# Optimization experiments

Measured on AMD Instinct MI355X. Metric: run time of the kernel, lower is better.

Reference implementation:

```python
import jax, jax.numpy as jnp
import numpy as np

N_EMBED = 1024
HEAD_SIZE = 64


def setup_inputs() -> dict:
    key = jax.random.key(0)
    kx, kq, kk, kv = jax.random.split(key, 4)
    x = jax.random.normal(kx, (8, 2048, N_EMBED), dtype=jnp.float32)
    s = 1.0 / np.sqrt(N_EMBED)
    # nn.Linear weights are [out, in]; store as [in, out] for x @ W
    W_q = jax.random.uniform(kq, (N_EMBED, HEAD_SIZE), jnp.float32, -s, s)
    W_k = jax.random.uniform(kk, (N_EMBED, HEAD_SIZE), jnp.float32, -s, s)
    W_v = jax.random.uniform(kv, (N_EMBED, HEAD_SIZE), jnp.float32, -s, s)
    return {"x": x, "W_q": W_q, "W_k": W_k, "W_v": W_v}


def reference(x, W_q, W_k, W_v):
    b, t, c = x.shape
    q = x @ W_q  # [b, t, h]
    k = x @ W_k
    v = x @ W_v
    scale = k.shape[-1] ** -0.5
    wei = jnp.einsum("bqh,bkh->bqk", q, k) * scale  # [b, t, t]
    causal = jnp.tril(jnp.ones((t, t), dtype=bool))
    wei = jnp.where(causal, wei, -jnp.inf)
    wei = jax.nn.softmax(wei, axis=-1)
    # dropout p=0.0 -> identity
    return jnp.einsum("bqk,bkh->bqh", wei, v)
```

## Files before the change

### kernel.cpp

```cpp
#include <hip/hip_runtime.h>
#include <math.h>

typedef unsigned short u16;
typedef unsigned int u32;
typedef __attribute__((ext_vector_type(4))) float f32x4;
typedef __attribute__((ext_vector_type(8))) short s16x8;
typedef __attribute__((ext_vector_type(4))) unsigned short u16x4;

#define T_ 2048
#define C_ 1024

__device__ __forceinline__ u16 f2b(float f) {
  u32 u = __builtin_bit_cast(u32, f);
  return (u16)((u + 0x8000u) >> 16);
}

__device__ __forceinline__ s16x8 pack8v(f32x4 a, f32x4 b) {
  s16x8 r;
  r[0] = (short)f2b(a[0]); r[1] = (short)f2b(a[1]);
  r[2] = (short)f2b(a[2]); r[3] = (short)f2b(a[3]);
  r[4] = (short)f2b(b[0]); r[5] = (short)f2b(b[1]);
  r[6] = (short)f2b(b[2]); r[7] = (short)f2b(b[3]);
  return r;
}

__device__ __forceinline__ void gld_lds16(const void* g, void* l) {
  __builtin_amdgcn_global_load_lds(
      (const __attribute__((address_space(1))) u32*)g,
      (__attribute__((address_space(3))) u32*)l, 16, 0, 0);
}

__global__ __launch_bounds__(256) void wconv(const float* __restrict__ Wq,
                                             const float* __restrict__ Wk,
                                             const float* __restrict__ Wv,
                                             u16* __restrict__ Wt) {
  __shared__ u16 t[64][68];
  const int bm = blockIdx.x >> 4;
  const int kt = blockIdx.x & 15;
  const float* src = (bm == 0) ? Wq : ((bm == 1) ? Wk : Wv);
  const float scale = (bm == 0) ? 0.18033688f : 1.0f;
  const int krow = threadIdx.x >> 2;
  const int c0 = (threadIdx.x & 3) * 16;
  const float* sp = src + (size_t)(kt * 64 + krow) * 64 + c0;
#pragma unroll
  for (int i = 0; i < 4; ++i) {
    float4 v = *(const float4*)(sp + i * 4);
    t[c0 + i * 4 + 0][krow] = f2b(v.x * scale);
    t[c0 + i * 4 + 1][krow] = f2b(v.y * scale);
    t[c0 + i * 4 + 2][krow] = f2b(v.z * scale);
    t[c0 + i * 4 + 3][krow] = f2b(v.w * scale);
  }
  __syncthreads();
  const int n = threadIdx.x >> 2;
  const int koff = (threadIdx.x & 3) * 16;
  u16* dst = Wt + (size_t)(bm * 64 + n) * C_ + kt * 64 + koff;
#pragma unroll
  for (int i = 0; i < 4; ++i)
    *(u16x4*)(dst + i * 4) = *(const u16x4*)(&t[n][koff + i * 4]);
}

__global__ __launch_bounds__(256, 2) void proj(const float* __restrict__ x,
                                               const u16* __restrict__ Wt,
                                               u16* __restrict__ qo,
                                               u16* __restrict__ ko,
                                               u16* __restrict__ vt) {
  __shared__ __align__(16) float xs[32 * 64];
  __shared__ __align__(16) u16 wsh[192 * 64];
  const int tid = threadIdx.x;
  const int wave = tid >> 6, lane = tid & 63;
  const int quad = lane >> 4, l15 = lane & 15;
  const int mg = wave >> 1, nh = wave & 1;
  const int m0 = blockIdx.x * 32;

  const int xrow_in = lane >> 4;
  const int xslot = lane & 15;
  const int wrow_in = lane >> 3;
  const int wg = (lane & 7) ^ wrow_in;

  f32x4 acc[6];
#pragma unroll
  for (int j = 0; j < 6; ++j) acc[j] = {0.f, 0.f, 0.f, 0.f};

  for (int kt = 0; kt < 16; ++kt) {
#pragma unroll
    for (int c = 0; c < 2; ++c) {
      const int row = 8 * wave + 4 * c + xrow_in;
      const int g = xslot ^ (row & 15);
      gld_lds16(x + (size_t)(m0 + row) * C_ + kt * 64 + g * 4,
                &xs[(8 * wave + 4 * c) * 64]);
    }
#pragma unroll
    for (int c = 0; c < 6; ++c) {
      const int row = (6 * wave + c) * 8 + wrow_in;
      gld_lds16(Wt + (size_t)row * C_ + kt * 64 + wg * 8,
                &wsh[(6 * wave + c) * 8 * 64]);
    }
    __syncthreads();
    s16x8 af[2];
#pragma unroll
    for (int ks = 0; ks < 2; ++ks) {
      const int row = 16 * mg + l15;
      const int cc = ks * 8 + quad * 2;
      f32x4 p0 = *(const f32x4*)&xs[row * 64 + ((cc ^ (row & 15)) * 4)];
      f32x4 p1 = *(const f32x4*)&xs[row * 64 + (((cc + 1) ^ (row & 15)) * 4)];
      af[ks] = pack8v(p0, p1);
    }
#pragma unroll
    for (int jj = 0; jj < 6; ++jj) {
      const int row = (nh * 6 + jj) * 16 + l15;
#pragma unroll
      for (int ks = 0; ks < 2; ++ks) {
        const int cc = ks * 4 + quad;
        s16x8 bf = *(const s16x8*)&wsh[row * 64 + ((cc ^ (row & 7)) * 8)];
        acc[jj] = __builtin_amdgcn_mfma_f32_16x16x32_bf16(af[ks], bf, acc[jj], 0, 0, 0);
      }
    }
    __syncthreads();
  }

  const int r0 = m0 + 16 * mg + quad * 4;
#pragma unroll
  for (int jj = 0; jj < 6; ++jj) {
    const int ns = nh * 6 + jj;
    if (ns < 4) {
      const int col = ns * 16 + l15;
#pragma unroll
      for (int i = 0; i < 4; ++i)
        qo[(size_t)(r0 + i) * 64 + col] = f2b(acc[jj][i]);
    } else if (ns < 8) {
      const int col = (ns - 4) * 16 + l15;
#pragma unroll
      for (int i = 0; i < 4; ++i)
        ko[(size_t)(r0 + i) * 64 + col] = f2b(acc[jj][i]);
    } else {
      const int d = (ns - 8) * 16 + l15;
      const int bb = r0 >> 11, t0 = r0 & 2047;
      u16x4 pk = {f2b(acc[jj][0]), f2b(acc[jj][1]), f2b(acc[jj][2]), f2b(acc[jj][3])};
      *(u16x4*)(vt + (size_t)bb * (64 * T_) + (size_t)d * T_ + t0) = pk;
    }
  }
}

__global__ __launch_bounds__(256, 4) void attn(const u16* __restrict__ qw,
                                               const u16* __restrict__ kw,
                                               const u16* __restrict__ vt,
                                               float* __restrict__ out) {
  __shared__ __align__(16) u16 Pb[4][16 * 72];
  __shared__ float mbuf[4][16];
  __shared__ float lbuf[4][16];
  const int tid = threadIdx.x;
  const int wave = tid >> 6, lane = tid & 63;
  const int quad = lane >> 4, l15 = lane & 15;
  const int b = blockIdx.x & 7;
  const int qt = 127 - (blockIdx.x >> 3);

  const u16* qp = qw + ((size_t)b * T_ + qt * 16) * 64;
  const u16* kb = kw + (size_t)b * T_ * 64;
  const u16* vb = vt + (size_t)b * 64 * T_;

  s16x8 qf[2];
#pragma unroll
  for (int ks = 0; ks < 2; ++ks)
    qf[ks] = *(const s16x8*)(qp + l15 * 64 + ks * 32 + quad * 8);

  f32x4 o[4];
#pragma unroll
  for (int m = 0; m < 4; ++m) o[m] = {0.f, 0.f, 0.f, 0.f};
  float mr = -INFINITY, lr = 0.0f;

  u16* P = Pb[wave];
  const int jd = qt >> 2;

  for (int j = wave; j <= jd; j += 4) {
    const u16* kp = kb + (size_t)j * 64 * 64;
    const u16* vp = vb + j * 64;
    s16x8 kf[2][4], vf[2][4];
#pragma unroll
    for (int ks = 0; ks < 2; ++ks)
#pragma unroll
      for (int m = 0; m < 4; ++m)
        kf[ks][m] = *(const s16x8*)(kp + (16 * m + l15) * 64 + ks * 32 + quad * 8);
#pragma unroll
    for (int ks = 0; ks < 2; ++ks)
#pragma unroll
      for (int m = 0; m < 4; ++m)
        vf[ks][m] = *(const s16x8*)(vp + (size_t)(16 * m + l15) * T_ + ks * 32 + quad * 8);

    f32x4 s[4];
#pragma unroll
    for (int m = 0; m < 4; ++m) s[m] = {0.f, 0.f, 0.f, 0.f};
#pragma unroll
    for (int ks = 0; ks < 2; ++ks)
#pragma unroll
      for (int m = 0; m < 4; ++m)
        s[m] = __builtin_amdgcn_mfma_f32_16x16x32_bf16(kf[ks][m], qf[ks], s[m], 0, 0, 0);

    if (j == jd) {
#pragma unroll
      for (int m = 0; m < 4; ++m)
#pragma unroll
        for (int i = 0; i < 4; ++i)
          if (64 * jd + 16 * m + quad * 4 + i > 16 * qt + l15) s[m][i] = -INFINITY;
    }
    float mt = s[0][0];
#pragma unroll
    for (int m = 0; m < 4; ++m)
#pragma unroll
      for (int i = 0; i < 4; ++i) mt = fmaxf(mt, s[m][i]);
    mt = fmaxf(mt, __shfl_xor(mt, 16));
    mt = fmaxf(mt, __shfl_xor(mt, 32));
    const float mn = fmaxf(mr, mt);
    const float al = exp2f(mr - mn);
    mr = mn;
    float rs = 0.0f;
#pragma unroll
    for (int m = 0; m < 4; ++m)
#pragma unroll
      for (int i = 0; i < 4; ++i) {
        float p = exp2f(s[m][i] - mn);
        s[m][i] = p;
        rs += p;
      }
    rs += __shfl_xor(rs, 16);
    rs += __shfl_xor(rs, 32);
    lr = lr * al + rs;
#pragma unroll
    for (int m = 0; m < 4; ++m) {
      u16x4 pk = {f2b(s[m][0]), f2b(s[m][1]), f2b(s[m][2]), f2b(s[m][3])};
      *(u16x4*)(&P[l15 * 72 + 16 * m + quad * 4]) = pk;
    }
#pragma unroll
    for (int m = 0; m < 4; ++m) o[m] *= al;
#pragma unroll
    for (int ks = 0; ks < 2; ++ks) {
      s16x8 pf = *(const s16x8*)(&P[l15 * 72 + ks * 32 + quad * 8]);
#pragma unroll
      for (int m = 0; m < 4; ++m)
        o[m] = __builtin_amdgcn_mfma_f32_16x16x32_bf16(vf[ks][m], pf, o[m], 0, 0, 0);
    }
  }
  if (quad == 0) {
    mbuf[wave][l15] = mr;
    lbuf[wave][l15] = lr;
  }
#pragma unroll
  for (int m = 0; m < 4; ++m) {
    u16x4 pk = {f2b(o[m][0]), f2b(o[m][1]), f2b(o[m][2]), f2b(o[m][3])};
    *(u16x4*)(&Pb[wave][l15 * 72 + 16 * m + quad * 4]) = pk;
  }
  __syncthreads();
  const int r = tid >> 4;
  const int cg = (tid & 15) * 4;
  float fw[4];
  float mstar = -INFINITY, lsum = 0.0f;
#pragma unroll
  for (int w = 0; w < 4; ++w) mstar = fmaxf(mstar, mbuf[w][r]);
#pragma unroll
  for (int w = 0; w < 4; ++w) {
    fw[w] = exp2f(mbuf[w][r] - mstar);
    lsum += fw[w] * lbuf[w][r];
  }
  const float inv = 1.0f / lsum;
  float a0 = 0.f, a1 = 0.f, a2 = 0.f, a3 = 0.f;
#pragma unroll
  for (int w = 0; w < 4; ++w) {
    u16x4 vv = *(const u16x4*)(&Pb[w][r * 72 + cg]);
    a0 += fw[w] * __builtin_bit_cast(float, ((u32)vv[0]) << 16);
    a1 += fw[w] * __builtin_bit_cast(float, ((u32)vv[1]) << 16);
    a2 += fw[w] * __builtin_bit_cast(float, ((u32)vv[2]) << 16);
    a3 += fw[w] * __builtin_bit_cast(float, ((u32)vv[3]) << 16);
  }
  float4 st = {a0 * inv, a1 * inv, a2 * inv, a3 * inv};
  *(float4*)(out + ((size_t)b * T_ + qt * 16 + r) * 64 + cg) = st;
}

extern "C" void kernel_launch(void* const* d_in, const int* in_sizes, int n_in,
                              void* d_out, int out_size, void* d_ws, size_t ws_size,
                              hipStream_t stream) {
  const float* x  = (const float*)d_in[0];
  const float* Wq = (const float*)d_in[1];
  const float* Wk = (const float*)d_in[2];
  const float* Wv = (const float*)d_in[3];
  float* out = (float*)d_out;
  char* ws = (char*)d_ws;
  u16* Wt = (u16*)ws;
  u16* q  = (u16*)(ws + 393216);
  u16* k  = (u16*)(ws + 393216 + 2097152);
  u16* vT = (u16*)(ws + 393216 + 2 * 2097152);
  hipLaunchKernelGGL(wconv, dim3(48), dim3(256), 0, stream, Wq, Wk, Wv, Wt);
  hipLaunchKernelGGL(proj, dim3(512), dim3(256), 0, stream, x, Wt, q, k, vT);
  hipLaunchKernelGGL(attn, dim3(1024), dim3(256), 0, stream, q, k, vT, out);
}
```

Measured before the change: 151.8 us.

## Double-buffer projection and restructure attention into split-KV with LDS-staged tiles and merge

The projection kernel now uses 512-thread blocks over 64 rows, converts x to bf16 once into LDS, and double-buffers both the x and W tiles so the next k-tile loads while MFMAs run. The attention kernel now gives each block 64 queries (one 16-row slice per wave) and stages shared K/V tiles into double-buffered LDS. The KV range is split into two halves per query tile, and a new merge kernel combines the two partial outputs. This is meant to reduce redundant global K/V loads and balance the causal workload, at the cost of an extra launch and a round trip of fp32 partials through global memory.

```diff
diff --git a/kernel.cpp b/kernel.cpp
--- a/kernel.cpp
+++ b/kernel.cpp
@@ -15,12 +15,12 @@
   return (u16)((u + 0x8000u) >> 16);
 }
 
-__device__ __forceinline__ s16x8 pack8v(f32x4 a, f32x4 b) {
+__device__ __forceinline__ s16x8 pack8(float4 a, float4 b) {
   s16x8 r;
-  r[0] = (short)f2b(a[0]); r[1] = (short)f2b(a[1]);
-  r[2] = (short)f2b(a[2]); r[3] = (short)f2b(a[3]);
-  r[4] = (short)f2b(b[0]); r[5] = (short)f2b(b[1]);
-  r[6] = (short)f2b(b[2]); r[7] = (short)f2b(b[3]);
+  r[0] = (short)f2b(a.x); r[1] = (short)f2b(a.y);
+  r[2] = (short)f2b(a.z); r[3] = (short)f2b(a.w);
+  r[4] = (short)f2b(b.x); r[5] = (short)f2b(b.y);
+  r[6] = (short)f2b(b.z); r[7] = (short)f2b(b.w);
   return r;
 }
 
@@ -59,62 +59,75 @@
     *(u16x4*)(dst + i * 4) = *(const u16x4*)(&t[n][koff + i * 4]);
 }
 
-__global__ __launch_bounds__(256, 2) void proj(const float* __restrict__ x,
+__global__ __launch_bounds__(512, 2) void proj(const float* __restrict__ x,
                                                const u16* __restrict__ Wt,
                                                u16* __restrict__ qo,
                                                u16* __restrict__ ko,
                                                u16* __restrict__ vt) {
-  __shared__ __align__(16) float xs[32 * 64];
-  __shared__ __align__(16) u16 wsh[192 * 64];
+  __shared__ __align__(16) u16 xs[2][64 * 64];
+  __shared__ __align__(16) u16 wsh[2][192 * 64];
   const int tid = threadIdx.x;
   const int wave = tid >> 6, lane = tid & 63;
   const int quad = lane >> 4, l15 = lane & 15;
   const int mg = wave >> 1, nh = wave & 1;
-  const int m0 = blockIdx.x * 32;
-
-  const int xrow_in = lane >> 4;
-  const int xslot = lane & 15;
-  const int wrow_in = lane >> 3;
-  const int wg = (lane & 7) ^ wrow_in;
+  const int m0 = blockIdx.x * 64;
+
+  const int rin = lane >> 3, slot = lane & 7;
+  const int xrow = tid >> 3, xcg = (tid & 7) * 8;
+  const float* xp = x + (size_t)(m0 + xrow) * C_ + xcg;
+  const int xslot = (tid & 7) ^ (xrow & 7);
+
+  auto stageW = [&](int kt, int buf) {
+#pragma unroll
+    for (int c = 0; c < 3; ++c) {
+      const int row0 = 24 * wave + 8 * c;
+      const int g = slot ^ rin;
+      gld_lds16(Wt + (size_t)(row0 + rin) * C_ + kt * 64 + g * 8,
+                &wsh[buf][row0 * 64]);
+    }
+  };
 
   f32x4 acc[6];
 #pragma unroll
   for (int j = 0; j < 6; ++j) acc[j] = {0.f, 0.f, 0.f, 0.f};
 
+  stageW(0, 0);
+  {
+    float4 p0 = *(const float4*)(xp);
+    float4 p1 = *(const float4*)(xp + 4);
+    *(s16x8*)(&xs[0][xrow * 64 + xslot * 8]) = pack8(p0, p1);
+  }
+  __syncthreads();
+
   for (int kt = 0; kt < 16; ++kt) {
-#pragma unroll
-    for (int c = 0; c < 2; ++c) {
-      const int row = 8 * wave + 4 * c + xrow_in;
-      const int g = xslot ^ (row & 15);
-      gld_lds16(x + (size_t)(m0 + row) * C_ + kt * 64 + g * 4,
-                &xs[(8 * wave + 4 * c) * 64]);
-    }
-#pragma unroll
-    for (int c = 0; c < 6; ++c) {
-      const int row = (6 * wave + c) * 8 + wrow_in;
-      gld_lds16(Wt + (size_t)row * C_ + kt * 64 + wg * 8,
-                &wsh[(6 * wave + c) * 8 * 64]);
-    }
-    __syncthreads();
+    const int buf = kt & 1;
+    float4 p0, p1;
+    if (kt < 15) {
+      stageW(kt + 1, buf ^ 1);
+      p0 = *(const float4*)(xp + (kt + 1) * 64);
+      p1 = *(const float4*)(xp + (kt + 1) * 64 + 4);
+    }
     s16x8 af[2];
-#pragma unroll
-    for (int ks = 0; ks < 2; ++ks) {
-      const int row = 16 * mg + l15;
-      const int cc = ks * 8 + quad * 2;
-      f32x4 p0 = *(const f32x4*)&xs[row * 64 + ((cc ^ (row & 15)) * 4)];
-      f32x4 p1 = *(const f32x4*)&xs[row * 64 + (((cc + 1) ^ (row & 15)) * 4)];
-      af[ks] = pack8v(p0, p1);
+    {
+      const int r = 16 * mg + l15;
+#pragma unroll
+      for (int ks = 0; ks < 2; ++ks) {
+        const int sl = (ks * 4 + quad) ^ (l15 & 7);
+        af[ks] = *(const s16x8*)&xs[buf][r * 64 + sl * 8];
+      }
     }
 #pragma unroll
     for (int jj = 0; jj < 6; ++jj) {
-      const int row = (nh * 6 + jj) * 16 + l15;
+      const int R = (nh * 6 + jj) * 16 + l15;
 #pragma unroll
       for (int ks = 0; ks < 2; ++ks) {
-        const int cc = ks * 4 + quad;
-        s16x8 bf = *(const s16x8*)&wsh[row * 64 + ((cc ^ (row & 7)) * 8)];
+        const int sl = (ks * 4 + quad) ^ (l15 & 7);
+        s16x8 bf = *(const s16x8*)&wsh[buf][R * 64 + sl * 8];
         acc[jj] = __builtin_amdgcn_mfma_f32_16x16x32_bf16(af[ks], bf, acc[jj], 0, 0, 0);
       }
     }
+    if (kt < 15)
+      *(s16x8*)(&xs[buf ^ 1][xrow * 64 + xslot * 8]) = pack8(p0, p1);
     __syncthreads();
   }
 
@@ -141,23 +154,27 @@
   }
 }
 
-__global__ __launch_bounds__(256, 4) void attn(const u16* __restrict__ qw,
+__global__ __launch_bounds__(256, 2) void attn(const u16* __restrict__ qw,
                                                const u16* __restrict__ kw,
                                                const u16* __restrict__ vt,
-                                               float* __restrict__ out) {
+                                               float* __restrict__ opart,
+                                               float2* __restrict__ ml) {
+  __shared__ __align__(16) u16 kvb[2][2][4096];
   __shared__ __align__(16) u16 Pb[4][16 * 72];
-  __shared__ float mbuf[4][16];
-  __shared__ float lbuf[4][16];
   const int tid = threadIdx.x;
   const int wave = tid >> 6, lane = tid & 63;
   const int quad = lane >> 4, l15 = lane & 15;
   const int b = blockIdx.x & 7;
-  const int qt = 127 - (blockIdx.x >> 3);
-
-  const u16* qp = qw + ((size_t)b * T_ + qt * 16) * 64;
+  const int h = (blockIdx.x >> 3) & 1;
+  const int qt = 31 - (blockIdx.x >> 4);
+
+  const u16* qp = qw + ((size_t)b * T_ + qt * 64 + 16 * wave) * 64;
   const u16* kb = kw + (size_t)b * T_ * 64;
   const u16* vb = vt + (size_t)b * 64 * T_;
 
+  const int n = qt + 1, c = (n + 1) >> 1;
+  const int j0 = h ? c : 0, j1 = h ? n : c;
+
   s16x8 qf[2];
 #pragma unroll
   for (int ks = 0; ks < 2; ++ks)
@@ -166,112 +183,131 @@
   f32x4 o[4];
 #pragma unroll
   for (int m = 0; m < 4; ++m) o[m] = {0.f, 0.f, 0.f, 0.f};
-  float mr = -INFINITY, lr = 0.0f;
-
+  float mr = -1e30f, lr = 0.0f;
+
+  const int rin = lane >> 3, slot = lane & 7;
+  const int g8 = slot ^ rin;
   u16* P = Pb[wave];
-  const int jd = qt >> 2;
-
-  for (int j = wave; j <= jd; j += 4) {
-    const u16* kp = kb + (size_t)j * 64 * 64;
-    const u16* vp = vb + j * 64;
-    s16x8 kf[2][4], vf[2][4];
-#pragma unroll
-    for (int ks = 0; ks < 2; ++ks)
+
+  auto stage = [&](int j, int buf) {
+    if (wave < 2) {
+#pragma unroll
+      for (int cc = 0; cc < 4; ++cc) {
+        const int r0 = 32 * wave + 8 * cc;
+        gld_lds16(kb + (size_t)(64 * j + r0 + rin) * 64 + g8 * 8,
+                  &kvb[buf][0][r0 * 64]);
+      }
+    } else {
+#pragma unroll
+      for (int cc = 0; cc < 4; ++cc) {
+        const int r0 = 32 * (wave - 2) + 8 * cc;
+        gld_lds16(vb + (size_t)(r0 + rin) * T_ + 64 * j + g8 * 8,
+                  &kvb[buf][1][r0 * 64]);
+      }
+    }
+  };
+
+  if (j0 < j1) {
+    stage(j0, 0);
+    __syncthreads();
+    for (int j = j0; j < j1; ++j) {
+      const int buf = (j - j0) & 1;
+      if (j + 1 < j1) stage(j + 1, buf ^ 1);
+      const u16* Kt = kvb[buf][0];
+      const u16* Vt = kvb[buf][1];
+      f32x4 s[4];
+#pragma unroll
+      for (int m = 0; m < 4; ++m) s[m] = {0.f, 0.f, 0.f, 0.f};
+#pragma unroll
+      for (int ks = 0; ks < 2; ++ks)
+#pragma unroll
+        for (int m = 0; m < 4; ++m) {
+          const int row = 16 * m + l15;
+          const int sl = (ks * 4 + quad) ^ (l15 & 7);
+          s16x8 kf = *(const s16x8*)&Kt[row * 64 + sl * 8];
+          s[m] = __builtin_amdgcn_mfma_f32_16x16x32_bf16(kf, qf[ks], s[m], 0, 0, 0);
+        }
+      if (j == qt) {
+#pragma unroll
+        for (int m = 0; m < 4; ++m)
+#pragma unroll
+          for (int i = 0; i < 4; ++i)
+            if (16 * m + quad * 4 + i > 16 * wave + l15) s[m][i] = -INFINITY;
+      }
+      float mt = s[0][0];
 #pragma unroll
       for (int m = 0; m < 4; ++m)
-        kf[ks][m] = *(const s16x8*)(kp + (16 * m + l15) * 64 + ks * 32 + quad * 8);
-#pragma unroll
-    for (int ks = 0; ks < 2; ++ks)
+#pragma unroll
+        for (int i = 0; i < 4; ++i) mt = fmaxf(mt, s[m][i]);
+      mt = fmaxf(mt, __shfl_xor(mt, 16));
+      mt = fmaxf(mt, __shfl_xor(mt, 32));
+      const float mn = fmaxf(mr, mt);
+      const float al = exp2f(mr - mn);
+      mr = mn;
+      float rs = 0.0f;
 #pragma unroll
       for (int m = 0; m < 4; ++m)
-        vf[ks][m] = *(const s16x8*)(vp + (size_t)(16 * m + l15) * T_ + ks * 32 + quad * 8);
-
-    f32x4 s[4];
-#pragma unroll
-    for (int m = 0; m < 4; ++m) s[m] = {0.f, 0.f, 0.f, 0.f};
-#pragma unroll
-    for (int ks = 0; ks < 2; ++ks)
-#pragma unroll
-      for (int m = 0; m < 4; ++m)
-        s[m] = __builtin_amdgcn_mfma_f32_16x16x32_bf16(kf[ks][m], qf[ks], s[m], 0, 0, 0);
-
-    if (j == jd) {
-#pragma unroll
-      for (int m = 0; m < 4; ++m)
-#pragma unroll
-        for (int i = 0; i < 4; ++i)
-          if (64 * jd + 16 * m + quad * 4 + i > 16 * qt + l15) s[m][i] = -INFINITY;
-    }
-    float mt = s[0][0];
-#pragma unroll
-    for (int m = 0; m < 4; ++m)
-#pragma unroll
-      for (int i = 0; i < 4; ++i) mt = fmaxf(mt, s[m][i]);
-    mt = fmaxf(mt, __shfl_xor(mt, 16));
-    mt = fmaxf(mt, __shfl_xor(mt, 32));
-    const float mn = fmaxf(mr, mt);
-    const float al = exp2f(mr - mn);
-    mr = mn;
-    float rs = 0.0f;
-#pragma unroll
-    for (int m = 0; m < 4; ++m)
-#pragma unroll
-      for (int i = 0; i < 4; ++i) {
-        float p = exp2f(s[m][i] - mn);
-        s[m][i] = p;
-        rs += p;
-      }
-    rs += __shfl_xor(rs, 16);
-    rs += __shfl_xor(rs, 32);
-    lr = lr * al + rs;
-#pragma unroll
-    for (int m = 0; m < 4; ++m) {
-      u16x4 pk = {f2b(s[m][0]), f2b(s[m][1]), f2b(s[m][2]), f2b(s[m][3])};
-      *(u16x4*)(&P[l15 * 72 + 16 * m + quad * 4]) = pk;
-    }
-#pragma unroll
-    for (int m = 0; m < 4; ++m) o[m] *= al;
-#pragma unroll
-    for (int ks = 0; ks < 2; ++ks) {
-      s16x8 pf = *(const s16x8*)(&P[l15 * 72 + ks * 32 + quad * 8]);
-#pragma unroll
-      for (int m = 0; m < 4; ++m)
-        o[m] = __builtin_amdgcn_mfma_f32_16x16x32_bf16(vf[ks][m], pf, o[m], 0, 0, 0);
-    }
-  }
-  if (quad == 0) {
-    mbuf[wave][l15] = mr;
-    lbuf[wave][l15] = lr;
-  }
-#pragma unroll
-  for (int m = 0; m < 4; ++m) {
-    u16x4 pk = {f2b(o[m][0]), f2b(o[m][1]), f2b(o[m][2]), f2b(o[m][3])};
-    *(u16x4*)(&Pb[wave][l15 * 72 + 16 * m + quad * 4]) = pk;
-  }
-  __syncthreads();
-  const int r = tid >> 4;
-  const int cg = (tid & 15) * 4;
-  float fw[4];
-  float mstar = -INFINITY, lsum = 0.0f;
-#pragma unroll
-  for (int w = 0; w < 4; ++w) mstar = fmaxf(mstar, mbuf[w][r]);
-#pragma unroll
-  for (int w = 0; w < 4; ++w) {
-    fw[w] = exp2f(mbuf[w][r] - mstar);
-    lsum += fw[w] * lbuf[w][r];
-  }
-  const float inv = 1.0f / lsum;
-  float a0 = 0.f, a1 = 0.f, a2 = 0.f, a3 = 0.f;
-#pragma unroll
-  for (int w = 0; w < 4; ++w) {
-    u16x4 vv = *(const u16x4*)(&Pb[w][r * 72 + cg]);
-    a0 += fw[w] * __builtin_bit_cast(float, ((u32)vv[0]) << 16);
-    a1 += fw[w] * __builtin_bit_cast(float, ((u32)vv[1]) << 16);
-    a2 += fw[w] * __builtin_bit_cast(float, ((u32)vv[2]) << 16);
-    a3 += fw[w] * __builtin_bit_cast(float, ((u32)vv[3]) << 16);
-  }
-  float4 st = {a0 * inv, a1 * inv, a2 * inv, a3 * inv};
-  *(float4*)(out + ((size_t)b * T_ + qt * 16 + r) * 64 + cg) = st;
+#pragma unroll
+        for (int i = 0; i < 4; ++i) {
+          float p = exp2f(s[m][i] - mn);
+          s[m][i] = p;
+          rs += p;
+        }
+      rs += __shfl_xor(rs, 16);
+      rs += __shfl_xor(rs, 32);
+      lr = lr * al + rs;
+#pragma unroll
+      for (int m = 0; m < 4; ++m) {
+        u16x4 pk = {f2b(s[m][0]), f2b(s[m][1]), f2b(s[m][2]), f2b(s[m][3])};
+        *(u16x4*)(&P[l15 * 72 + 16 * m + quad * 4]) = pk;
+      }
+#pragma unroll
+      for (int m = 0; m < 4; ++m) o[m] *= al;
+#pragma unroll
+      for (int ks = 0; ks < 2; ++ks) {
+        s16x8 pf = *(const s16x8*)(&P[l15 * 72 + ks * 32 + quad * 8]);
+#pragma unroll
+        for (int m = 0; m < 4; ++m) {
+          const int row = 16 * m + l15;
+          const int sl = (ks * 4 + quad) ^ (l15 & 7);
+          s16x8 vf = *(const s16x8*)&Vt[row * 64 + sl * 8];
+          o[m] = __builtin_amdgcn_mfma_f32_16x16x32_bf16(vf, pf, o[m], 0, 0, 0);
+        }
+      }
+      __syncthreads();
+    }
+  }
+  const int pidx = ((b * 32 + qt) * 2 + h);
+  float* OP = opart + (size_t)pidx * 4096;
+  const int qloc = 16 * wave + l15;
+#pragma unroll
+  for (int m = 0; m < 4; ++m)
+    *(f32x4*)(&OP[qloc * 64 + 16 * m + quad * 4]) = o[m];
+  if (quad == 0) ml[pidx * 64 + qloc] = {mr, lr};
+}
+
+__global__ __launch_bounds__(256) void merge(const float* __restrict__ opart,
+                                             const float2* __restrict__ ml,
+                                             float* __restrict__ out) {
+  const int blk = blockIdx.x;
+  const int b = blk >> 5, qt = blk & 31;
+  const int t = threadIdx.x;
+  const int r = t >> 2, cg = (t & 3) * 16;
+  const float2 ml0 = ml[(blk * 2 + 0) * 64 + r];
+  const float2 ml1 = ml[(blk * 2 + 1) * 64 + r];
+  const float mstar = fmaxf(ml0.x, ml1.x);
+  const float f0 = exp2f(ml0.x - mstar), f1 = exp2f(ml1.x - mstar);
+  const float inv = 1.0f / (f0 * ml0.y + f1 * ml1.y);
+  const float* O0 = opart + (size_t)(blk * 2 + 0) * 4096 + r * 64 + cg;
+  const float* O1 = opart + (size_t)(blk * 2 + 1) * 4096 + r * 64 + cg;
+  float* op = out + ((size_t)b * T_ + qt * 64 + r) * 64 + cg;
+#pragma unroll
+  for (int e = 0; e < 16; e += 4) {
+    f32x4 a = *(const f32x4*)(O0 + e);
+    f32x4 bb = *(const f32x4*)(O1 + e);
+    f32x4 rv = (a * f0 + bb * f1) * inv;
+    *(f32x4*)(op + e) = rv;
+  }
 }
 
 extern "C" void kernel_launch(void* const* d_in, const int* in_sizes, int n_in,
@@ -285,9 +321,12 @@
   char* ws = (char*)d_ws;
   u16* Wt = (u16*)ws;
   u16* q  = (u16*)(ws + 393216);
-  u16* k  = (u16*)(ws + 393216 + 2097152);
-  u16* vT = (u16*)(ws + 393216 + 2 * 2097152);
+  u16* k  = (u16*)(ws + 2490368);
+  u16* vT = (u16*)(ws + 4587520);
+  float*  OP = (float*)(ws + 6684672);
+  float2* ML = (float2*)(ws + 15073280);
   hipLaunchKernelGGL(wconv, dim3(48), dim3(256), 0, stream, Wq, Wk, Wv, Wt);
-  hipLaunchKernelGGL(proj, dim3(512), dim3(256), 0, stream, x, Wt, q, k, vT);
-  hipLaunchKernelGGL(attn, dim3(1024), dim3(256), 0, stream, q, k, vT, out);
-}
+  hipLaunchKernelGGL(proj, dim3(256), dim3(512), 0, stream, x, Wt, q, k, vT);
+  hipLaunchKernelGGL(attn, dim3(512), dim3(256), 0, stream, q, k, vT, OP, ML);
+  hipLaunchKernelGGL(merge, dim3(256), dim3(256), 0, stream, OP, ML, out);
+}
```

Measured after the change: 138.2 us. -9.0%, faster.
